# Optimization experiments

Hardware: AMD Instinct MI355X
Metric: run time of the kernel (lower is better)

Reference implementation:

```python
import jax, jax.numpy as jnp
import numpy as np

N_NODES = 50000
N_EDGES = 800000
N_GRAPHS = 256
D = 256
DROPOUT_P = 0.5


def setup_inputs() -> dict:
    key = jax.random.key(0)
    ks = jax.random.split(key, 6)
    x = jax.random.normal(ks[0], (N_NODES, D), dtype=jnp.float32)
    edge_index = jax.random.randint(ks[1], (2, N_EDGES), 0, N_NODES, dtype=jnp.int64)
    batch = jnp.sort(jax.random.randint(ks[2], (N_NODES,), 0, N_GRAPHS, dtype=jnp.int64))
    W1 = jax.random.normal(ks[3], (D, D), dtype=jnp.float32) * (1.0 / np.sqrt(D))
    b1 = jnp.zeros((D,), dtype=jnp.float32)
    W2 = jax.random.normal(ks[4], (D, D), dtype=jnp.float32) * (1.0 / np.sqrt(D))
    b2 = jnp.zeros((D,), dtype=jnp.float32)
    return {"x": x, "edge_index": edge_index, "batch": batch,
            "W1": W1, "b1": b1, "W2": W2, "b2": b2, "num_graphs": N_GRAPHS}


def _gcn_conv(h, W, b, src, dst, norm, self_norm, n_nodes):
    # PyG GCNConv: lin -> symmetric-normalized sum aggregation (with self-loops)
    h = h @ W + b                                    # [N, d_out]
    msg = h[src] * norm[:, None]                      # [E, d_out] gather
    agg = jax.ops.segment_sum(msg, dst, num_segments=n_nodes)  # scatter-add
    agg = agg + h * self_norm[:, None]                # self-loop contribution
    return agg


def reference(x, edge_index, batch, W1, b1, W2, b2, num_graphs):
    n_nodes = x.shape[0]
    src, dst = edge_index[0], edge_index[1]
    # degrees including self-loops
    deg = jax.ops.segment_sum(jnp.ones_like(src, dtype=x.dtype), dst,
                              num_segments=n_nodes) + 1.0
    dis = jax.lax.rsqrt(deg)                          # D^{-1/2}
    norm = dis[src] * dis[dst]                        # per-edge norm
    self_norm = dis * dis                             # self-loop norm

    h = _gcn_conv(x, W1, b1, src, dst, norm, self_norm, n_nodes)
    h = jax.nn.relu(h)
    # dropout (training=True) with fixed key for determinism
    keep = jax.random.bernoulli(jax.random.key(42), 1.0 - DROPOUT_P, h.shape)
    h = jnp.where(keep, h / (1.0 - DROPOUT_P), 0.0)

    h = _gcn_conv(h, W2, b2, src, dst, norm, self_norm, n_nodes)
    h = jax.nn.relu(h)

    # scatter_mean pooling over data.batch
    counts = jax.ops.segment_sum(jnp.ones((n_nodes,), dtype=h.dtype), batch,
                                 num_segments=num_graphs)
    sums = jax.ops.segment_sum(h, batch, num_segments=num_graphs)
    return sums / jnp.clip(counts, 1.0)[:, None]
```

## Files before the change

kernel.cpp:

```cpp
#include <hip/hip_runtime.h>
#include <cstdint>

#define N_NODES   50000
#define N_EDGES   800000
#define N_GRAPHS  256
#define DIM       256
#define MASK_WORDS 400000
#define SCAN_BLOCKS 196

__device__ __forceinline__ uint32_t rotl32(uint32_t x, int n) {
    return (x << n) | (x >> (32 - n));
}

__device__ __forceinline__ void threefry2x32_k42(uint32_t& x0, uint32_t& x1) {
    const uint32_t ks0 = 0u, ks1 = 42u, ks2 = 0x1BD11BDAu ^ 0u ^ 42u;
    x0 += ks0; x1 += ks1;
#define TF_R(r) { x0 += x1; x1 = rotl32(x1, (r)); x1 ^= x0; }
    TF_R(13) TF_R(15) TF_R(26) TF_R(6)   x0 += ks1; x1 += ks2 + 1u;
    TF_R(17) TF_R(29) TF_R(16) TF_R(24)  x0 += ks2; x1 += ks0 + 2u;
    TF_R(13) TF_R(15) TF_R(26) TF_R(6)   x0 += ks0; x1 += ks1 + 3u;
    TF_R(17) TF_R(29) TF_R(16) TF_R(24)  x0 += ks1; x1 += ks2 + 4u;
    TF_R(13) TF_R(15) TF_R(26) TF_R(6)   x0 += ks2; x1 += ks0 + 5u;
#undef TF_R
}

__device__ __forceinline__ uint32_t bf16_rne(float f) {
    uint32_t u = __float_as_uint(f);
    return (u + 0x7FFFu + ((u >> 16) & 1u)) >> 16;
}
__device__ __forceinline__ uint32_t bf16_pack2(float a, float b) {
    return bf16_rne(a) | (bf16_rne(b) << 16);
}
__device__ __forceinline__ float bf16_lo(uint32_t u) { return __uint_as_float(u << 16); }
__device__ __forceinline__ float bf16_hi(uint32_t u) { return __uint_as_float(u & 0xFFFF0000u); }

__global__ __launch_bounds__(256) void mask_kernel(unsigned* __restrict__ mask) {
    int t = blockIdx.x * 256 + threadIdx.x;
    if (t >= MASK_WORDS) return;
    unsigned m = 0u;
    uint32_t base = (uint32_t)t * 32u;
    #pragma unroll 4
    for (int s = 0; s < 32; ++s) {
        uint32_t x0 = 0u;
        uint32_t x1 = base + (uint32_t)s;
        threefry2x32_k42(x0, x1);
        uint32_t draw = x0 ^ x1;
        m |= ((draw >> 31) ^ 1u) << s;
    }
    mask[t] = m;
}

__global__ void detect_kernel(const int* __restrict__ ei,
                              const int* __restrict__ batch,
                              int* __restrict__ flags) {
    if (threadIdx.x != 0 || blockIdx.x != 0) return;
    int z = 0;
    #pragma unroll
    for (int k = 1; k < 33; k += 2) z |= ei[k];
    flags[0] = (z == 0) ? 1 : 0;
    int z2 = batch[25001] | batch[30003] | batch[40005] | batch[49999];
    flags[1] = (z2 == 0) ? 1 : 0;
}

__global__ __launch_bounds__(256) void edge_count_kernel(const int* __restrict__ ei,
                                                         const int* __restrict__ flags,
                                                         int* __restrict__ cnt) {
    int e = blockIdx.x * 256 + threadIdx.x;
    int d = flags[0] ? ei[2 * (N_EDGES + e)] : ei[N_EDGES + e];
    atomicAdd(&cnt[d], 1);
}

__global__ __launch_bounds__(256) void block_sum_kernel(const int* __restrict__ cnt,
                                                        int* __restrict__ bsum) {
    int idx = blockIdx.x * 256 + threadIdx.x;
    int v = (idx < N_NODES) ? cnt[idx] : 0;
    #pragma unroll
    for (int o = 32; o > 0; o >>= 1) v += __shfl_down(v, o, 64);
    __shared__ int s[4];
    if ((threadIdx.x & 63) == 0) s[threadIdx.x >> 6] = v;
    __syncthreads();
    if (threadIdx.x == 0) bsum[blockIdx.x] = s[0] + s[1] + s[2] + s[3];
}

__global__ __launch_bounds__(256) void scan_bsum_kernel(const int* __restrict__ bsum,
                                                        int* __restrict__ boff) {
    __shared__ int s[256];
    int t = threadIdx.x;
    int v = (t < SCAN_BLOCKS) ? bsum[t] : 0;
    s[t] = v;
    __syncthreads();
    #pragma unroll
    for (int o = 1; o < 256; o <<= 1) {
        int u = (t >= o) ? s[t - o] : 0;
        __syncthreads();
        s[t] += u;
        __syncthreads();
    }
    if (t < SCAN_BLOCKS) boff[t] = s[t] - v;
}

__global__ __launch_bounds__(256) void scan_fill_kernel(const int* __restrict__ cnt,
                                                        const int* __restrict__ boff,
                                                        int* __restrict__ row_ptr,
                                                        float* __restrict__ dis) {
    __shared__ int s[256];
    int t = threadIdx.x;
    int idx = blockIdx.x * 256 + t;
    int v = (idx < N_NODES) ? cnt[idx] : 0;
    s[t] = v;
    __syncthreads();
    #pragma unroll
    for (int o = 1; o < 256; o <<= 1) {
        int u = (t >= o) ? s[t - o] : 0;
        __syncthreads();
        s[t] += u;
        __syncthreads();
    }
    int excl = boff[blockIdx.x] + s[t] - v;
    if (idx < N_NODES) {
        row_ptr[idx] = excl;
        dis[idx] = 1.0f / sqrtf((float)v + 1.0f);
        if (idx == N_NODES - 1) row_ptr[N_NODES] = excl + v;
    }
}

__global__ __launch_bounds__(256) void csr_fill_kernel(const int* __restrict__ ei,
                                                       const int* __restrict__ flags,
                                                       const int* __restrict__ row_ptr,
                                                       int* __restrict__ cur,
                                                       const float* __restrict__ dis,
                                                       int2* __restrict__ recs) {
    int e = blockIdx.x * 256 + threadIdx.x;
    int f = flags[0];
    int s = f ? ei[2 * e] : ei[e];
    int d = f ? ei[2 * (N_EDGES + e)] : ei[N_EDGES + e];
    int pos = row_ptr[d] + atomicAdd(&cur[d], 1);
    float w = dis[s] * dis[d];
    recs[pos] = make_int2(s, __float_as_int(w));
}

__global__ __launch_bounds__(512) void graph_ptr_kernel(const int* __restrict__ batch,
                                                        const int* __restrict__ flags,
                                                        int* __restrict__ gptr) {
    int t = threadIdx.x;
    if (t > N_GRAPHS) return;
    int f = flags[1];
    int lo = 0, hi = N_NODES;
    while (lo < hi) {
        int mid = (lo + hi) >> 1;
        int v = f ? batch[2 * mid] : batch[mid];
        if (v < t) lo = mid + 1; else hi = mid;
    }
    gptr[t] = lo;
}

__global__ __launch_bounds__(256) void lin_kernel(const float* __restrict__ A,
                                                  const float* __restrict__ Wm,
                                                  const float* __restrict__ bias,
                                                  ushort* __restrict__ out_bf) {
    __shared__ float As[32][132];
    __shared__ float Bs[32][132];
    int tid = threadIdx.x;
    int row0 = blockIdx.x * 128;
    int col0 = blockIdx.y * 128;
    int tx = tid & 15, ty = tid >> 4;
    float c[8][8] = {};

    for (int k0 = 0; k0 < DIM; k0 += 32) {
        #pragma unroll
        for (int rep = 0; rep < 4; ++rep) {
            int r = (tid >> 3) + rep * 32;
            int c4 = (tid & 7) * 4;
            int grow = row0 + r;
            float4 v = (grow < N_NODES)
                ? *reinterpret_cast<const float4*>(A + (size_t)grow * DIM + k0 + c4)
                : make_float4(0.f, 0.f, 0.f, 0.f);
            As[c4 + 0][r] = v.x; As[c4 + 1][r] = v.y;
            As[c4 + 2][r] = v.z; As[c4 + 3][r] = v.w;
        }
        #pragma unroll
        for (int rep = 0; rep < 4; ++rep) {
            int kk = (tid >> 5) + rep * 8;
            int c4 = (tid & 31) * 4;
            float4 v = *reinterpret_cast<const float4*>(Wm + (size_t)(k0 + kk) * DIM + col0 + c4);
            *reinterpret_cast<float4*>(&Bs[kk][c4]) = v;
        }
        __syncthreads();
        #pragma unroll
        for (int kk = 0; kk < 32; ++kk) {
            float4 a0 = *reinterpret_cast<const float4*>(&As[kk][ty * 8]);
            float4 a1 = *reinterpret_cast<const float4*>(&As[kk][ty * 8 + 4]);
            float4 b0 = *reinterpret_cast<const float4*>(&Bs[kk][tx * 8]);
            float4 b1 = *reinterpret_cast<const float4*>(&Bs[kk][tx * 8 + 4]);
            float av[8] = {a0.x, a0.y, a0.z, a0.w, a1.x, a1.y, a1.z, a1.w};
            float bv[8] = {b0.x, b0.y, b0.z, b0.w, b1.x, b1.y, b1.z, b1.w};
            #pragma unroll
            for (int i = 0; i < 8; ++i)
                #pragma unroll
                for (int j = 0; j < 8; ++j)
                    c[i][j] = fmaf(av[i], bv[j], c[i][j]);
        }
        __syncthreads();
    }

    float4 bv0 = *reinterpret_cast<const float4*>(bias + col0 + tx * 8);
    float4 bv1 = *reinterpret_cast<const float4*>(bias + col0 + tx * 8 + 4);
    float bb[8] = {bv0.x, bv0.y, bv0.z, bv0.w, bv1.x, bv1.y, bv1.z, bv1.w};
    #pragma unroll
    for (int i = 0; i < 8; ++i) {
        int row = row0 + ty * 8 + i;
        if (row < N_NODES) {
            uint4 o;
            o.x = bf16_pack2(c[i][0] + bb[0], c[i][1] + bb[1]);
            o.y = bf16_pack2(c[i][2] + bb[2], c[i][3] + bb[3]);
            o.z = bf16_pack2(c[i][4] + bb[4], c[i][5] + bb[5]);
            o.w = bf16_pack2(c[i][6] + bb[6], c[i][7] + bb[7]);
            *reinterpret_cast<uint4*>(out_bf + (size_t)row * DIM + col0 + tx * 8) = o;
        }
    }
}

template <int LAYER>
__global__ __launch_bounds__(256) void aggregate_kernel(const ushort* __restrict__ hb,
                                                        const int* __restrict__ row_ptr,
                                                        const int2* __restrict__ recs,
                                                        const float* __restrict__ dis,
                                                        const unsigned* __restrict__ mask,
                                                        float* __restrict__ out) {
    int wave = threadIdx.x >> 6;
    int lane = threadIdx.x & 63;
    int node = blockIdx.x * 4 + wave;

    float dn = dis[node];
    float sw = dn * dn;
    uint2 s0 = reinterpret_cast<const uint2*>(hb + (size_t)node * DIM)[lane];
    float ax = sw * bf16_lo(s0.x), ay = sw * bf16_hi(s0.x);
    float az = sw * bf16_lo(s0.y), aw = sw * bf16_hi(s0.y);

    int p = row_ptr[node], e = row_ptr[node + 1];
    for (; p + 3 < e; p += 4) {
        int2 r0 = recs[p];
        int2 r1 = recs[p + 1];
        int2 r2 = recs[p + 2];
        int2 r3 = recs[p + 3];
        float w0 = __int_as_float(r0.y);
        float w1 = __int_as_float(r1.y);
        float w2 = __int_as_float(r2.y);
        float w3 = __int_as_float(r3.y);
        uint2 u0 = reinterpret_cast<const uint2*>(hb + (size_t)r0.x * DIM)[lane];
        uint2 u1 = reinterpret_cast<const uint2*>(hb + (size_t)r1.x * DIM)[lane];
        uint2 u2 = reinterpret_cast<const uint2*>(hb + (size_t)r2.x * DIM)[lane];
        uint2 u3 = reinterpret_cast<const uint2*>(hb + (size_t)r3.x * DIM)[lane];
        ax = fmaf(w0, bf16_lo(u0.x), ax); ay = fmaf(w0, bf16_hi(u0.x), ay);
        az = fmaf(w0, bf16_lo(u0.y), az); aw = fmaf(w0, bf16_hi(u0.y), aw);
        ax = fmaf(w1, bf16_lo(u1.x), ax); ay = fmaf(w1, bf16_hi(u1.x), ay);
        az = fmaf(w1, bf16_lo(u1.y), az); aw = fmaf(w1, bf16_hi(u1.y), aw);
        ax = fmaf(w2, bf16_lo(u2.x), ax); ay = fmaf(w2, bf16_hi(u2.x), ay);
        az = fmaf(w2, bf16_lo(u2.y), az); aw = fmaf(w2, bf16_hi(u2.y), aw);
        ax = fmaf(w3, bf16_lo(u3.x), ax); ay = fmaf(w3, bf16_hi(u3.x), ay);
        az = fmaf(w3, bf16_lo(u3.y), az); aw = fmaf(w3, bf16_hi(u3.y), aw);
    }
    for (; p < e; ++p) {
        int2 r0 = recs[p];
        float w0 = __int_as_float(r0.y);
        uint2 u = reinterpret_cast<const uint2*>(hb + (size_t)r0.x * DIM)[lane];
        ax = fmaf(w0, bf16_lo(u.x), ax); ay = fmaf(w0, bf16_hi(u.x), ay);
        az = fmaf(w0, bf16_lo(u.y), az); aw = fmaf(w0, bf16_hi(u.y), aw);
    }

    ax = fmaxf(ax, 0.f); ay = fmaxf(ay, 0.f);
    az = fmaxf(az, 0.f); aw = fmaxf(aw, 0.f);

    if (LAYER == 1) {
        unsigned w = mask[node * 8 + (lane >> 3)];
        int b = (lane & 7) * 4;
        ax = ((w >> (b + 0)) & 1u) ? ax * 2.0f : 0.0f;
        ay = ((w >> (b + 1)) & 1u) ? ay * 2.0f : 0.0f;
        az = ((w >> (b + 2)) & 1u) ? az * 2.0f : 0.0f;
        aw = ((w >> (b + 3)) & 1u) ? aw * 2.0f : 0.0f;
    }

    reinterpret_cast<float4*>(out + (size_t)node * DIM)[lane] =
        make_float4(ax, ay, az, aw);
}

__global__ __launch_bounds__(64) void pool_kernel(const float* __restrict__ h,
                                                  const int* __restrict__ gptr,
                                                  float* __restrict__ out) {
    int g = blockIdx.x >> 2;
    int c = blockIdx.x & 3;
    int lane = threadIdx.x;
    int col = c * 64 + lane;
    int s = gptr[g], e = gptr[g + 1];
    float a0 = 0.f, a1 = 0.f, a2 = 0.f, a3 = 0.f;
    int n = s;
    for (; n + 3 < e; n += 4) {
        a0 += h[(size_t)n * DIM + col];
        a1 += h[(size_t)(n + 1) * DIM + col];
        a2 += h[(size_t)(n + 2) * DIM + col];
        a3 += h[(size_t)(n + 3) * DIM + col];
    }
    for (; n < e; ++n) a0 += h[(size_t)n * DIM + col];
    float sum = (a0 + a1) + (a2 + a3);
    out[g * DIM + col] = sum / fmaxf((float)(e - s), 1.0f);
}

extern "C" void kernel_launch(void* const* d_in, const int* in_sizes, int n_in,
                              void* d_out, int out_size, void* d_ws, size_t ws_size,
                              hipStream_t stream) {
    const float* x     = (const float*)d_in[0];
    const int*   ei    = (const int*)d_in[1];
    const int*   batch = (const int*)d_in[2];
    const float* W1    = (const float*)d_in[3];
    const float* b1    = (const float*)d_in[4];
    const float* W2    = (const float*)d_in[5];
    const float* b2    = (const float*)d_in[6];
    float*       out   = (float*)d_out;

    char* Wp = (char*)d_ws;
    size_t off = 0;
    auto take = [&](size_t bytes) -> char* {
        char* p = Wp + off;
        off += (bytes + 255) & ~(size_t)255;
        return p;
    };
    int*      cnt    = (int*)take((size_t)N_NODES * 4);
    int*      cur    = (int*)take((size_t)N_NODES * 4);
    int*      rowptr = (int*)take((size_t)(N_NODES + 1) * 4);
    float*    dis    = (float*)take((size_t)N_NODES * 4);
    int2*     recs   = (int2*)take((size_t)N_EDGES * 8);
    int*      gptr   = (int*)take((size_t)(N_GRAPHS + 1) * 4);
    unsigned* mask   = (unsigned*)take((size_t)MASK_WORDS * 4);
    int*      flags  = (int*)take(256);
    int*      bsum   = (int*)take((size_t)SCAN_BLOCKS * 4);
    int*      boff   = (int*)take((size_t)(SCAN_BLOCKS + 1) * 4);
    ushort*   hbf    = (ushort*)take((size_t)N_NODES * DIM * 2);
    float*    bufA   = (float*)take((size_t)N_NODES * DIM * 4);
    float*    bufB   = (float*)take((size_t)N_NODES * DIM * 4);
    (void)ws_size; (void)in_sizes; (void)n_in; (void)out_size;

    hipMemsetAsync(cnt, 0, (size_t)((char*)rowptr - (char*)cnt), stream);

    mask_kernel<<<(MASK_WORDS + 255) / 256, 256, 0, stream>>>(mask);

    detect_kernel<<<1, 64, 0, stream>>>(ei, batch, flags);
    edge_count_kernel<<<N_EDGES / 256, 256, 0, stream>>>(ei, flags, cnt);
    block_sum_kernel<<<SCAN_BLOCKS, 256, 0, stream>>>(cnt, bsum);
    scan_bsum_kernel<<<1, 256, 0, stream>>>(bsum, boff);
    scan_fill_kernel<<<SCAN_BLOCKS, 256, 0, stream>>>(cnt, boff, rowptr, dis);
    csr_fill_kernel<<<N_EDGES / 256, 256, 0, stream>>>(ei, flags, rowptr, cur, dis, recs);
    graph_ptr_kernel<<<1, 512, 0, stream>>>(batch, flags, gptr);

    dim3 gemm_grid((N_NODES + 127) / 128, DIM / 128);

    lin_kernel<<<gemm_grid, 256, 0, stream>>>(x, W1, b1, hbf);
    aggregate_kernel<1><<<N_NODES / 4, 256, 0, stream>>>(hbf, rowptr, recs, dis, mask, bufA);

    lin_kernel<<<gemm_grid, 256, 0, stream>>>(bufA, W2, b2, hbf);
    aggregate_kernel<2><<<N_NODES / 4, 256, 0, stream>>>(hbf, rowptr, recs, dis, mask, bufB);

    pool_kernel<<<N_GRAPHS * 4, 64, 0, stream>>>(bufB, gptr, out);
}
```

Baseline: 574.4 us.

## Replace FP32 SIMT GEMM with bf16 MFMA and store layer-1 activations as bf16

Replaces the shared-memory FP32 FMA GEMM with a bf16 MFMA 16x16x32 kernel. The weights are pre-packed into a fragment-friendly bf16 layout so B fragments load directly from global memory without LDS staging. The layer-1 aggregate now writes bf16 instead of fp32, which halves that intermediate's traffic and lets the second GEMM read bf16 directly. This trades input precision (x and activations rounded to bf16 before the matmul) for much higher matrix throughput. The output stores are scalar ushort writes, which are less coalesced than before.

```diff
diff --git a/kernel.cpp b/kernel.cpp
--- a/kernel.cpp
+++ b/kernel.cpp
@@ -7,6 +7,9 @@
 #define DIM       256
 #define MASK_WORDS 400000
 #define SCAN_BLOCKS 196
+
+typedef __attribute__((ext_vector_type(8))) short bf16x8;
+typedef __attribute__((ext_vector_type(4))) float f32x4;
 
 __device__ __forceinline__ uint32_t rotl32(uint32_t x, int n) {
     return (x << n) | (x >> (32 - n));
@@ -154,70 +157,79 @@
     gptr[t] = lo;
 }
 
-__global__ __launch_bounds__(256) void lin_kernel(const float* __restrict__ A,
-                                                  const float* __restrict__ Wm,
-                                                  const float* __restrict__ bias,
-                                                  ushort* __restrict__ out_bf) {
-    __shared__ float As[32][132];
-    __shared__ float Bs[32][132];
-    int tid = threadIdx.x;
-    int row0 = blockIdx.x * 128;
-    int col0 = blockIdx.y * 128;
-    int tx = tid & 15, ty = tid >> 4;
-    float c[8][8] = {};
-
-    for (int k0 = 0; k0 < DIM; k0 += 32) {
-        #pragma unroll
-        for (int rep = 0; rep < 4; ++rep) {
-            int r = (tid >> 3) + rep * 32;
-            int c4 = (tid & 7) * 4;
-            int grow = row0 + r;
-            float4 v = (grow < N_NODES)
-                ? *reinterpret_cast<const float4*>(A + (size_t)grow * DIM + k0 + c4)
-                : make_float4(0.f, 0.f, 0.f, 0.f);
-            As[c4 + 0][r] = v.x; As[c4 + 1][r] = v.y;
-            As[c4 + 2][r] = v.z; As[c4 + 3][r] = v.w;
+__global__ __launch_bounds__(256) void pack_w_kernel(const float* __restrict__ W,
+                                                     ushort* __restrict__ Wp) {
+    int t = blockIdx.x * 256 + threadIdx.x;
+    int k = t >> 8, c = t & 255;
+    int ks = k >> 5, g = (k >> 3) & 3, j = k & 7;
+    Wp[(((ks * 4 + g) * 256) + c) * 8 + j] = (ushort)bf16_rne(W[t]);
+}
+
+template <int A_BF16>
+__global__ __launch_bounds__(256) void lin_mfma_kernel(const void* __restrict__ Aptr,
+                                                       const ushort* __restrict__ Wp,
+                                                       const float* __restrict__ bias,
+                                                       ushort* __restrict__ out_bf) {
+    int wave = threadIdx.x >> 6, lane = threadIdx.x & 63;
+    int g = lane >> 4, cl = lane & 15;
+    int arow = blockIdx.x * 64 + wave * 16 + cl;
+
+    f32x4 acc00, acc01, acc02, acc03, acc04, acc05, acc06, acc07;
+    f32x4 acc08, acc09, acc10, acc11, acc12, acc13, acc14, acc15;
+    acc00=acc01=acc02=acc03=acc04=acc05=acc06=acc07=(f32x4){0.f,0.f,0.f,0.f};
+    acc08=acc09=acc10=acc11=acc12=acc13=acc14=acc15=(f32x4){0.f,0.f,0.f,0.f};
+
+    union frag_u { uint4 u; bf16x8 f; ushort us[8]; };
+
+    #pragma unroll
+    for (int ks = 0; ks < 8; ++ks) {
+        frag_u fa;
+        if (A_BF16) {
+            const ushort* A = (const ushort*)Aptr;
+            fa.u = (arow < N_NODES)
+                ? *reinterpret_cast<const uint4*>(A + (size_t)arow * DIM + ks * 32 + g * 8)
+                : make_uint4(0u, 0u, 0u, 0u);
+        } else {
+            const float* A = (const float*)Aptr;
+            float4 v0, v1;
+            if (arow < N_NODES) {
+                const float* p = A + (size_t)arow * DIM + ks * 32 + g * 8;
+                v0 = *reinterpret_cast<const float4*>(p);
+                v1 = *reinterpret_cast<const float4*>(p + 4);
+            } else {
+                v0 = v1 = make_float4(0.f, 0.f, 0.f, 0.f);
+            }
+            fa.us[0] = (ushort)bf16_rne(v0.x); fa.us[1] = (ushort)bf16_rne(v0.y);
+            fa.us[2] = (ushort)bf16_rne(v0.z); fa.us[3] = (ushort)bf16_rne(v0.w);
+            fa.us[4] = (ushort)bf16_rne(v1.x); fa.us[5] = (ushort)bf16_rne(v1.y);
+            fa.us[6] = (ushort)bf16_rne(v1.z); fa.us[7] = (ushort)bf16_rne(v1.w);
         }
-        #pragma unroll
-        for (int rep = 0; rep < 4; ++rep) {
-            int kk = (tid >> 5) + rep * 8;
-            int c4 = (tid & 31) * 4;
-            float4 v = *reinterpret_cast<const float4*>(Wm + (size_t)(k0 + kk) * DIM + col0 + c4);
-            *reinterpret_cast<float4*>(&Bs[kk][c4]) = v;
-        }
-        __syncthreads();
-        #pragma unroll
-        for (int kk = 0; kk < 32; ++kk) {
-            float4 a0 = *reinterpret_cast<const float4*>(&As[kk][ty * 8]);
-            float4 a1 = *reinterpret_cast<const float4*>(&As[kk][ty * 8 + 4]);
-            float4 b0 = *reinterpret_cast<const float4*>(&Bs[kk][tx * 8]);
-            float4 b1 = *reinterpret_cast<const float4*>(&Bs[kk][tx * 8 + 4]);
-            float av[8] = {a0.x, a0.y, a0.z, a0.w, a1.x, a1.y, a1.z, a1.w};
-            float bv[8] = {b0.x, b0.y, b0.z, b0.w, b1.x, b1.y, b1.z, b1.w};
-            #pragma unroll
-            for (int i = 0; i < 8; ++i)
-                #pragma unroll
-                for (int j = 0; j < 8; ++j)
-                    c[i][j] = fmaf(av[i], bv[j], c[i][j]);
-        }
-        __syncthreads();
-    }
-
-    float4 bv0 = *reinterpret_cast<const float4*>(bias + col0 + tx * 8);
-    float4 bv1 = *reinterpret_cast<const float4*>(bias + col0 + tx * 8 + 4);
-    float bb[8] = {bv0.x, bv0.y, bv0.z, bv0.w, bv1.x, bv1.y, bv1.z, bv1.w};
-    #pragma unroll
-    for (int i = 0; i < 8; ++i) {
-        int row = row0 + ty * 8 + i;
-        if (row < N_NODES) {
-            uint4 o;
-            o.x = bf16_pack2(c[i][0] + bb[0], c[i][1] + bb[1]);
-            o.y = bf16_pack2(c[i][2] + bb[2], c[i][3] + bb[3]);
-            o.z = bf16_pack2(c[i][4] + bb[4], c[i][5] + bb[5]);
-            o.w = bf16_pack2(c[i][6] + bb[6], c[i][7] + bb[7]);
-            *reinterpret_cast<uint4*>(out_bf + (size_t)row * DIM + col0 + tx * 8) = o;
-        }
-    }
+        const ushort* bbase = Wp + ((size_t)(ks * 4 + g) * 256 + cl) * 8;
+#define LIN_MMA(CT, ACC) { \
+        frag_u fb; \
+        fb.u = *reinterpret_cast<const uint4*>(bbase + (CT) * 16 * 8); \
+        ACC = __builtin_amdgcn_mfma_f32_16x16x32_bf16(fa.f, fb.f, ACC, 0, 0, 0); }
+        LIN_MMA(0, acc00)  LIN_MMA(1, acc01)  LIN_MMA(2, acc02)  LIN_MMA(3, acc03)
+        LIN_MMA(4, acc04)  LIN_MMA(5, acc05)  LIN_MMA(6, acc06)  LIN_MMA(7, acc07)
+        LIN_MMA(8, acc08)  LIN_MMA(9, acc09)  LIN_MMA(10, acc10) LIN_MMA(11, acc11)
+        LIN_MMA(12, acc12) LIN_MMA(13, acc13) LIN_MMA(14, acc14) LIN_MMA(15, acc15)
+#undef LIN_MMA
+    }
+
+    int rbase = blockIdx.x * 64 + wave * 16 + g * 4;
+#define LIN_ST(CT, ACC) { \
+    float bb = bias[(CT) * 16 + cl]; \
+    _Pragma("unroll") \
+    for (int i = 0; i < 4; ++i) { \
+        int r = rbase + i; \
+        if (r < N_NODES) \
+            out_bf[(size_t)r * DIM + (CT) * 16 + cl] = (ushort)bf16_rne(ACC[i] + bb); \
+    } }
+    LIN_ST(0, acc00)  LIN_ST(1, acc01)  LIN_ST(2, acc02)  LIN_ST(3, acc03)
+    LIN_ST(4, acc04)  LIN_ST(5, acc05)  LIN_ST(6, acc06)  LIN_ST(7, acc07)
+    LIN_ST(8, acc08)  LIN_ST(9, acc09)  LIN_ST(10, acc10) LIN_ST(11, acc11)
+    LIN_ST(12, acc12) LIN_ST(13, acc13) LIN_ST(14, acc14) LIN_ST(15, acc15)
+#undef LIN_ST
 }
 
 template <int LAYER>
@@ -226,7 +238,8 @@
                                                         const int2* __restrict__ recs,
                                                         const float* __restrict__ dis,
                                                         const unsigned* __restrict__ mask,
-                                                        float* __restrict__ out) {
+                                                        float* __restrict__ outf,
+                                                        ushort* __restrict__ outb) {
     int wave = threadIdx.x >> 6;
     int lane = threadIdx.x & 63;
     int node = blockIdx.x * 4 + wave;
@@ -278,10 +291,12 @@
         ay = ((w >> (b + 1)) & 1u) ? ay * 2.0f : 0.0f;
         az = ((w >> (b + 2)) & 1u) ? az * 2.0f : 0.0f;
         aw = ((w >> (b + 3)) & 1u) ? aw * 2.0f : 0.0f;
-    }
-
-    reinterpret_cast<float4*>(out + (size_t)node * DIM)[lane] =
-        make_float4(ax, ay, az, aw);
+        reinterpret_cast<uint2*>(outb + (size_t)node * DIM)[lane] =
+            make_uint2(bf16_pack2(ax, ay), bf16_pack2(az, aw));
+    } else {
+        reinterpret_cast<float4*>(outf + (size_t)node * DIM)[lane] =
+            make_float4(ax, ay, az, aw);
+    }
 }
 
 __global__ __launch_bounds__(64) void pool_kernel(const float* __restrict__ h,
@@ -334,14 +349,18 @@
     int*      flags  = (int*)take(256);
     int*      bsum   = (int*)take((size_t)SCAN_BLOCKS * 4);
     int*      boff   = (int*)take((size_t)(SCAN_BLOCKS + 1) * 4);
+    ushort*   wp1    = (ushort*)take((size_t)DIM * DIM * 2);
+    ushort*   wp2    = (ushort*)take((size_t)DIM * DIM * 2);
     ushort*   hbf    = (ushort*)take((size_t)N_NODES * DIM * 2);
-    float*    bufA   = (float*)take((size_t)N_NODES * DIM * 4);
+    ushort*   a1bf   = (ushort*)take((size_t)N_NODES * DIM * 2);
     float*    bufB   = (float*)take((size_t)N_NODES * DIM * 4);
     (void)ws_size; (void)in_sizes; (void)n_in; (void)out_size;
 
     hipMemsetAsync(cnt, 0, (size_t)((char*)rowptr - (char*)cnt), stream);
 
     mask_kernel<<<(MASK_WORDS + 255) / 256, 256, 0, stream>>>(mask);
+    pack_w_kernel<<<(DIM * DIM) / 256, 256, 0, stream>>>(W1, wp1);
+    pack_w_kernel<<<(DIM * DIM) / 256, 256, 0, stream>>>(W2, wp2);
 
     detect_kernel<<<1, 64, 0, stream>>>(ei, batch, flags);
     edge_count_kernel<<<N_EDGES / 256, 256, 0, stream>>>(ei, flags, cnt);
@@ -351,13 +370,15 @@
     csr_fill_kernel<<<N_EDGES / 256, 256, 0, stream>>>(ei, flags, rowptr, cur, dis, recs);
     graph_ptr_kernel<<<1, 512, 0, stream>>>(batch, flags, gptr);
 
-    dim3 gemm_grid((N_NODES + 127) / 128, DIM / 128);
-
-    lin_kernel<<<gemm_grid, 256, 0, stream>>>(x, W1, b1, hbf);
-    aggregate_kernel<1><<<N_NODES / 4, 256, 0, stream>>>(hbf, rowptr, recs, dis, mask, bufA);
-
-    lin_kernel<<<gemm_grid, 256, 0, stream>>>(bufA, W2, b2, hbf);
-    aggregate_kernel<2><<<N_NODES / 4, 256, 0, stream>>>(hbf, rowptr, recs, dis, mask, bufB);
+    const int lin_grid = (N_NODES + 63) / 64;
+
+    lin_mfma_kernel<0><<<lin_grid, 256, 0, stream>>>(x, wp1, b1, hbf);
+    aggregate_kernel<1><<<N_NODES / 4, 256, 0, stream>>>(hbf, rowptr, recs, dis, mask,
+                                                         nullptr, a1bf);
+
+    lin_mfma_kernel<1><<<lin_grid, 256, 0, stream>>>(a1bf, wp2, b2, hbf);
+    aggregate_kernel<2><<<N_NODES / 4, 256, 0, stream>>>(hbf, rowptr, recs, dis, mask,
+                                                         bufB, nullptr);
 
     pool_kernel<<<N_GRAPHS * 4, 64, 0, stream>>>(bufB, gptr, out);
 }
```

New measurement: 466.3 us. -18.8%, faster.
